# Kernel optimization log

Measured on AMD Instinct MI355X. Metric: run time of the kernel, lower is better.

Reference implementation:

```python
import jax, jax.numpy as jnp
import numpy as np

EMBED_DIM = 1024
NUM_HEADS = 16
HEAD_DIM = EMBED_DIM // NUM_HEADS


def setup_inputs() -> dict:
    key = jax.random.key(0)
    ks = jax.random.split(key, 11)
    B, S, D = 2, 2048, EMBED_DIM
    s = 1.0 / np.sqrt(D)
    inp = {
        "query": jax.random.normal(ks[0], (B, S, D), jnp.float32),
        "key": jax.random.normal(ks[1], (B, S, D), jnp.float32),
        "value": jax.random.normal(ks[2], (B, S, D), jnp.float32),
        # torch Linear weights: [out, in]
        "Wq": jax.random.normal(ks[3], (D, D), jnp.float32) * s,
        "bq": jnp.zeros((D,), jnp.float32),
        "Wk": jax.random.normal(ks[4], (D, D), jnp.float32) * s,
        "bk": jnp.zeros((D,), jnp.float32),
        "Wv": jax.random.normal(ks[5], (D, D), jnp.float32) * s,
        "bv": jnp.zeros((D,), jnp.float32),
        "Wo": jax.random.normal(ks[6], (D, D), jnp.float32) * s,
        "bo": jnp.zeros((D,), jnp.float32),
    }
    return inp


def reference(query, key, value, Wq, bq, Wk, bk, Wv, bv, Wo, bo):
    B, Q, D = query.shape
    K = key.shape[1]
    H, Hd = NUM_HEADS, HEAD_DIM
    # NOTE: source divides by scaling = head_dim**-0.5, i.e. multiplies by sqrt(head_dim)
    scaling = float(Hd) ** (-0.5)

    q = (query @ Wq.T + bq).reshape(B, Q, H, Hd).transpose(0, 2, 1, 3)  # [B,H,Q,Hd]
    k = (key @ Wk.T + bk).reshape(B, K, H, Hd).transpose(0, 2, 1, 3)    # [B,H,K,Hd]
    v = (value @ Wv.T + bv).reshape(B, K, H, Hd).transpose(0, 2, 1, 3)  # [B,H,K,Hd]

    scores = jnp.einsum("bhqd,bhkd->bhqk", q, k) / scaling
    attn = jax.nn.softmax(scores, axis=-1)  # dropout=0 (eval)
    out = jnp.einsum("bhqk,bhkd->bhqd", attn, v)
    out = out.transpose(0, 2, 1, 3).reshape(B, Q, D)
    return out @ Wo.T + bo
```

## Files before the change

kernel.cpp:

```cpp
#include <hip/hip_runtime.h>
#include <type_traits>
#include <utility>

#define B_ 2
#define S_ 2048
#define D_ 1024
#define H_ 16
#define HD_ 64
#define KDIM 1024

typedef __attribute__((ext_vector_type(8))) short    s16x8;
typedef __attribute__((ext_vector_type(8))) _Float16 h16x8;
typedef __attribute__((ext_vector_type(4))) float    f32x4;
typedef __attribute__((ext_vector_type(4))) int      i32x4;
typedef __attribute__((ext_vector_type(2))) int      i32x2;

template <typename T, typename = void> struct mfma_takes : std::false_type {};
template <typename T>
struct mfma_takes<T, std::void_t<decltype(__builtin_amdgcn_mfma_f32_16x16x32_f16(
    std::declval<T>(), std::declval<T>(), std::declval<f32x4>(), 0, 0, 0))>>
    : std::true_type {};
using frag8 = std::conditional_t<mfma_takes<h16x8>::value, h16x8, s16x8>;

__device__ __forceinline__ f32x4 mfma_f16(frag8 a, frag8 b, f32x4 c) {
  return __builtin_amdgcn_mfma_f32_16x16x32_f16(a, b, c, 0, 0, 0);
}

__device__ __forceinline__ short f2h(float f) {
  _Float16 h = (_Float16)f;
  short s; __builtin_memcpy(&s, &h, 2);
  return s;
}
__device__ __forceinline__ frag8 ld_frag(const short* p) {
  return __builtin_bit_cast(frag8, *(const i32x4*)p);
}
__device__ __forceinline__ float fast_exp2(float x) {
  return __builtin_amdgcn_exp2f(x);
}

typedef __attribute__((address_space(1))) const void gvoid;
typedef __attribute__((address_space(3))) void lvoid;
__device__ __forceinline__ void async_copy16(const void* g, void* l) {
  __builtin_amdgcn_global_load_lds((gvoid*)g, (lvoid*)l, 16, 0, 0);
}

#define RAW_BARRIER() asm volatile("s_barrier" ::: "memory")
#define WAITCNT_VM(n) asm volatile("s_waitcnt vmcnt(" #n ")" ::: "memory")

__global__ __launch_bounds__(256)
void conv_all(const float* __restrict__ q, const float* __restrict__ k,
              const float* __restrict__ v, const float* __restrict__ Wq,
              const float* __restrict__ Wk, const float* __restrict__ Wv,
              const float* __restrict__ Wo,
              short* __restrict__ qh, short* __restrict__ kh,
              short* __restrict__ vh, short* __restrict__ wq,
              short* __restrict__ wk, short* __restrict__ wv,
              short* __restrict__ wo) {
  const int blk = blockIdx.x;
  const float* src; short* dst; int base;
  if (blk < 2048)      { src = q;  dst = qh; base = blk; }
  else if (blk < 4096) { src = k;  dst = kh; base = blk - 2048; }
  else if (blk < 6144) { src = v;  dst = vh; base = blk - 4096; }
  else if (blk < 6656) { src = Wq; dst = wq; base = blk - 6144; }
  else if (blk < 7168) { src = Wk; dst = wk; base = blk - 6656; }
  else if (blk < 7680) { src = Wv; dst = wv; base = blk - 7168; }
  else                 { src = Wo; dst = wo; base = blk - 7680; }
  const int i = base * 2048 + threadIdx.x * 8;
  float4 a0 = *(const float4*)(src + i);
  float4 a1 = *(const float4*)(src + i + 4);
  short h[8] = { f2h(a0.x), f2h(a0.y), f2h(a0.z), f2h(a0.w),
                 f2h(a1.x), f2h(a1.y), f2h(a1.z), f2h(a1.w) };
  i32x4 ph; __builtin_memcpy(&ph, h, 16);
  *(i32x4*)(dst + i) = ph;
}

template <int OUTK>
__device__ __forceinline__
void gemm_body(const short* __restrict__ Ap, const short* __restrict__ Wp,
               const float* __restrict__ bias, void* __restrict__ Out,
               float scale, int omode, short* As, short* Bs, int bm, int bn) {
  const int t = threadIdx.x, wave = t >> 6, lane = t & 63;
  const int laneN = lane & 15, quad = lane >> 4;
  const int wm = wave & 1, wn = wave >> 1;

  f32x4 acc[4][4];
#pragma unroll
  for (int i = 0; i < 4; ++i)
#pragma unroll
    for (int j = 0; j < 4; ++j)
#pragma unroll
      for (int r = 0; r < 4; ++r) acc[i][j][r] = 0.f;

  auto stage = [&](int buf, int kk) {
#pragma unroll
    for (int j = 0; j < 2; ++j) {
      const int chunk = j * 256 + t;
      const int row = chunk >> 2;
      const int g = (chunk & 3) ^ ((row >> 1) & 3);
      async_copy16(Ap + (size_t)(bm * 128 + row) * KDIM + kk + g * 8,
                   As + buf * 4096 + chunk * 8);
      async_copy16(Wp + (size_t)(bn * 128 + row) * KDIM + kk + g * 8,
                   Bs + buf * 4096 + chunk * 8);
    }
  };

  stage(0, 0);
  int buf = 0;
  for (int kk = 0; kk < KDIM; kk += 32, buf ^= 1) {
    if (kk + 32 < KDIM) {
      stage(buf ^ 1, kk + 32);
      WAITCNT_VM(4);
    } else {
      WAITCNT_VM(0);
    }
    RAW_BARRIER();

    frag8 aF[4], bF[4];
#pragma unroll
    for (int mi = 0; mi < 4; ++mi) {
      const int row = wm * 64 + mi * 16 + laneN;
      aF[mi] = ld_frag(As + buf * 4096 + row * 32 +
                       ((quad ^ ((row >> 1) & 3)) * 8));
    }
#pragma unroll
    for (int ni = 0; ni < 4; ++ni) {
      const int row = wn * 64 + ni * 16 + laneN;
      bF[ni] = ld_frag(Bs + buf * 4096 + row * 32 +
                       ((quad ^ ((row >> 1) & 3)) * 8));
    }
#pragma unroll
    for (int mi = 0; mi < 4; ++mi)
#pragma unroll
      for (int ni = 0; ni < 4; ++ni)
        acc[mi][ni] = mfma_f16(aF[mi], bF[ni], acc[mi][ni]);
    RAW_BARRIER();
  }

#pragma unroll
  for (int mi = 0; mi < 4; ++mi)
#pragma unroll
    for (int ni = 0; ni < 4; ++ni) {
      const int colg = bn * 128 + wn * 64 + ni * 16 + laneN;
      const float bb = bias[colg];
      if (OUTK == 1 && omode == 2) {
        const int rowg0 = bm * 128 + wm * 64 + mi * 16 + quad * 4;
        const int b = rowg0 >> 11, s0 = rowg0 & 2047;
        const int h = colg >> 6, hd = colg & 63;
        short pk[4];
#pragma unroll
        for (int r = 0; r < 4; ++r) pk[r] = f2h(acc[mi][ni][r] + bb);
        i32x2 w; __builtin_memcpy(&w, pk, 8);
        *(i32x2*)((short*)Out + (((size_t)(b * H_ + h)) * HD_ + hd) * S_ + s0) = w;
      } else {
#pragma unroll
        for (int r = 0; r < 4; ++r) {
          const int rowg = bm * 128 + wm * 64 + mi * 16 + quad * 4 + r;
          const float v = acc[mi][ni][r] + bb;
          if (OUTK == 0) {
            ((float*)Out)[(size_t)rowg * 1024 + colg] = v;
          } else {
            const int b = rowg >> 11, s = rowg & 2047;
            const int h = colg >> 6, hd = colg & 63;
            ((short*)Out)[(((size_t)(b * H_ + h)) * S_ + s) * HD_ + hd] =
                f2h(v * scale);
          }
        }
      }
    }
}

__global__ __launch_bounds__(256, 3)
void gemm_qkv(const short* __restrict__ qh, const short* __restrict__ kh,
              const short* __restrict__ vh, const short* __restrict__ wq,
              const short* __restrict__ wk, const short* __restrict__ wv,
              const float* __restrict__ bq, const float* __restrict__ bk,
              const float* __restrict__ bv, short* __restrict__ Qf,
              short* __restrict__ Kf, short* __restrict__ Vt, float QS) {
  __shared__ short As[2 * 4096];
  __shared__ short Bs[2 * 4096];
  const int z = blockIdx.z;
  const short* A = z == 0 ? qh : z == 1 ? kh : vh;
  const short* W = z == 0 ? wq : z == 1 ? wk : wv;
  const float* bias = z == 0 ? bq : z == 1 ? bk : bv;
  short* Out = z == 0 ? Qf : z == 1 ? Kf : Vt;
  gemm_body<1>(A, W, bias, Out, z == 0 ? QS : 1.0f, z == 2 ? 2 : 1,
               As, Bs, blockIdx.y, blockIdx.x);
}

__global__ __launch_bounds__(256, 3)
void gemm_out(const short* __restrict__ Ow, const short* __restrict__ wo,
              const float* __restrict__ bo, float* __restrict__ out) {
  __shared__ short As[2 * 4096];
  __shared__ short Bs[2 * 4096];
  gemm_body<0>(Ow, wo, bo, out, 1.0f, 0, As, Bs, blockIdx.y, blockIdx.x);
}

__global__ __launch_bounds__(512, 2)
void attn(const short* __restrict__ Qf, const short* __restrict__ Kf,
          const short* __restrict__ Vt_, short* __restrict__ Ow) {
  __shared__ short Ks[2 * 4096];
  __shared__ short Vts[2 * 4096];
  __shared__ short Ps[8][16 * 72];

  const int qt = blockIdx.x, h = blockIdx.y, b = blockIdx.z;
  const size_t head = ((size_t)b * H_ + h) * (size_t)S_ * HD_;

  const int t = threadIdx.x;
  const int wave = t >> 6, lane = t & 63;
  const int laneN = lane & 15, quad = lane >> 4;

  frag8 qf[2];
  {
    const size_t row = (size_t)qt * 128 + wave * 16 + laneN;
#pragma unroll
    for (int half = 0; half < 2; ++half)
      qf[half] = ld_frag(Qf + head + row * HD_ + half * 32 + quad * 8);
  }

  f32x4 o[4];
  float m_r = -1e30f, l_r = 0.f;
#pragma unroll
  for (int i = 0; i < 4; ++i)
#pragma unroll
    for (int j = 0; j < 4; ++j) o[i][j] = 0.f;

  auto stage = [&](int buf, int kt) {
    const int chunk = t;
    const int row = chunk >> 3;
    const int g = (chunk & 7) ^ (row & 7);
    const int ldsoff = buf * 4096 + chunk * 8;
    async_copy16(Kf + head + (size_t)(kt * 64 + row) * HD_ + g * 8, Ks + ldsoff);
    async_copy16(Vt_ + head + (size_t)row * S_ + kt * 64 + g * 8, Vts + ldsoff);
  };

  stage(0, 0);
  int buf = 0;
  for (int kt = 0; kt < 32; ++kt, buf ^= 1) {
    if (kt + 1 < 32) {
      stage(buf ^ 1, kt + 1);
      WAITCNT_VM(2);
    } else {
      WAITCNT_VM(0);
    }
    RAW_BARRIER();

    frag8 vf[4][2];
#pragma unroll
    for (int dt = 0; dt < 4; ++dt) {
      const int row = dt * 16 + laneN;
#pragma unroll
      for (int half = 0; half < 2; ++half)
        vf[dt][half] = ld_frag(Vts + buf * 4096 + row * 64 +
                               (((half * 4 + quad) ^ (row & 7)) * 8));
    }

    f32x4 s[4];
#pragma unroll
    for (int nt = 0; nt < 4; ++nt) {
      const int row = nt * 16 + laneN;
      const int o0 = buf * 4096 + row * 64 + ((quad ^ (row & 7)) * 8);
      const int o1 = buf * 4096 + row * 64 + (((quad + 4) ^ (row & 7)) * 8);
      frag8 k0 = ld_frag(Ks + o0), k1 = ld_frag(Ks + o1);
      f32x4 acc;
#pragma unroll
      for (int j = 0; j < 4; ++j) acc[j] = 0.f;
      acc = mfma_f16(k0, qf[0], acc);
      acc = mfma_f16(k1, qf[1], acc);
      s[nt] = acc;
    }

    {
      float mx = -1e30f;
#pragma unroll
      for (int nt = 0; nt < 4; ++nt)
#pragma unroll
        for (int r = 0; r < 4; ++r) mx = fmaxf(mx, s[nt][r]);
      mx = fmaxf(mx, __shfl_xor(mx, 16));
      mx = fmaxf(mx, __shfl_xor(mx, 32));
      const float mn = fmaxf(m_r, mx);
      const float al = fast_exp2(m_r - mn);
      m_r = mn;
      float rs = 0.f;
#pragma unroll
      for (int nt = 0; nt < 4; ++nt)
#pragma unroll
        for (int r = 0; r < 4; ++r) {
          const float p = fast_exp2(s[nt][r] - mn);
          s[nt][r] = p; rs += p;
        }
      rs += __shfl_xor(rs, 16);
      rs += __shfl_xor(rs, 32);
      l_r = l_r * al + rs;
#pragma unroll
      for (int dt = 0; dt < 4; ++dt)
#pragma unroll
        for (int r = 0; r < 4; ++r) o[dt][r] *= al;
    }

#pragma unroll
    for (int nt = 0; nt < 4; ++nt) {
      short pk[4] = { f2h(s[nt][0]), f2h(s[nt][1]),
                      f2h(s[nt][2]), f2h(s[nt][3]) };
      i32x2 w; __builtin_memcpy(&w, pk, 8);
      *(i32x2*)&Ps[wave][laneN * 72 + nt * 16 + quad * 4] = w;
    }
    const frag8 p0 = ld_frag(&Ps[wave][laneN * 72 + quad * 8]);
    const frag8 p1 = ld_frag(&Ps[wave][laneN * 72 + 32 + quad * 8]);
#pragma unroll
    for (int dt = 0; dt < 4; ++dt) {
      o[dt] = mfma_f16(vf[dt][0], p0, o[dt]);
      o[dt] = mfma_f16(vf[dt][1], p1, o[dt]);
    }
    RAW_BARRIER();
  }

  {
    const float inv = 1.0f / l_r;
    const int sg = qt * 128 + wave * 16 + laneN;
    short* dst = Ow + ((size_t)b * S_ + sg) * D_ + h * HD_;
#pragma unroll
    for (int dt = 0; dt < 4; ++dt) {
      short pk[4] = { f2h(o[dt][0] * inv), f2h(o[dt][1] * inv),
                      f2h(o[dt][2] * inv), f2h(o[dt][3] * inv) };
      i32x2 w; __builtin_memcpy(&w, pk, 8);
      *(i32x2*)(dst + dt * 16 + quad * 4) = w;
    }
  }
}

extern "C" void kernel_launch(void* const* d_in, const int* in_sizes, int n_in,
                              void* d_out, int out_size, void* d_ws, size_t ws_size,
                              hipStream_t stream) {
  const float* q  = (const float*)d_in[0];
  const float* k  = (const float*)d_in[1];
  const float* v  = (const float*)d_in[2];
  const float* Wq = (const float*)d_in[3];
  const float* bq = (const float*)d_in[4];
  const float* Wk = (const float*)d_in[5];
  const float* bk = (const float*)d_in[6];
  const float* Wv = (const float*)d_in[7];
  const float* bv = (const float*)d_in[8];
  const float* Wo = (const float*)d_in[9];
  const float* bo = (const float*)d_in[10];

  const size_t NTOK = (size_t)B_ * S_ * D_;
  const size_t NW   = (size_t)D_ * D_;
  short* p = (short*)d_ws;
  short* qh = p; p += NTOK;  short* kh = p; p += NTOK;  short* vh = p; p += NTOK;
  short* wq = p; p += NW;    short* wk = p; p += NW;
  short* wv = p; p += NW;    short* wo = p; p += NW;
  short* Qf = p; p += NTOK;  short* Kf = p; p += NTOK;
  short* Vt = p; p += NTOK;  short* Ow = p; p += NTOK;

  dim3 blk(256);

  conv_all<<<8192, blk, 0, stream>>>(q, k, v, Wq, Wk, Wv, Wo,
                                     qh, kh, vh, wq, wk, wv, wo);

  const float QS = 11.541560327111707f;
  dim3 gqkv(D_ / 128, (B_ * S_) / 128, 3);
  gemm_qkv<<<gqkv, blk, 0, stream>>>(qh, kh, vh, wq, wk, wv, bq, bk, bv,
                                     Qf, Kf, Vt, QS);

  attn<<<dim3(S_ / 128, H_, B_), dim3(512), 0, stream>>>(Qf, Kf, Vt, Ow);

  dim3 gg(D_ / 128, (B_ * S_) / 128);
  gemm_out<<<gg, blk, 0, stream>>>(Ow, wo, bo, (float*)d_out);
}
```

Baseline: 234.8 us.

## Fuse fp32-to-fp16 activation conversion into QKV GEMM and remap attention blocks per XCD

Measured after the change: 246.6 us. 1.05x slower.

```diff
diff --git a/kernel.cpp b/kernel.cpp
--- a/kernel.cpp
+++ b/kernel.cpp
@@ -34,6 +34,11 @@
 __device__ __forceinline__ frag8 ld_frag(const short* p) {
   return __builtin_bit_cast(frag8, *(const i32x4*)p);
 }
+__device__ __forceinline__ frag8 cvt_frag(f32x4 a, f32x4 b) {
+  _Float16 h[8] = { (_Float16)a[0], (_Float16)a[1], (_Float16)a[2], (_Float16)a[3],
+                    (_Float16)b[0], (_Float16)b[1], (_Float16)b[2], (_Float16)b[3] };
+  frag8 f; __builtin_memcpy(&f, h, 16); return f;
+}
 __device__ __forceinline__ float fast_exp2(float x) {
   return __builtin_amdgcn_exp2f(x);
 }
@@ -48,23 +53,16 @@
 #define WAITCNT_VM(n) asm volatile("s_waitcnt vmcnt(" #n ")" ::: "memory")
 
 __global__ __launch_bounds__(256)
-void conv_all(const float* __restrict__ q, const float* __restrict__ k,
-              const float* __restrict__ v, const float* __restrict__ Wq,
-              const float* __restrict__ Wk, const float* __restrict__ Wv,
-              const float* __restrict__ Wo,
-              short* __restrict__ qh, short* __restrict__ kh,
-              short* __restrict__ vh, short* __restrict__ wq,
-              short* __restrict__ wk, short* __restrict__ wv,
-              short* __restrict__ wo) {
+void conv_w(const float* __restrict__ Wq, const float* __restrict__ Wk,
+            const float* __restrict__ Wv, const float* __restrict__ Wo,
+            short* __restrict__ wq, short* __restrict__ wk,
+            short* __restrict__ wv, short* __restrict__ wo) {
   const int blk = blockIdx.x;
   const float* src; short* dst; int base;
-  if (blk < 2048)      { src = q;  dst = qh; base = blk; }
-  else if (blk < 4096) { src = k;  dst = kh; base = blk - 2048; }
-  else if (blk < 6144) { src = v;  dst = vh; base = blk - 4096; }
-  else if (blk < 6656) { src = Wq; dst = wq; base = blk - 6144; }
-  else if (blk < 7168) { src = Wk; dst = wk; base = blk - 6656; }
-  else if (blk < 7680) { src = Wv; dst = wv; base = blk - 7168; }
-  else                 { src = Wo; dst = wo; base = blk - 7680; }
+  if (blk < 512)       { src = Wq; dst = wq; base = blk; }
+  else if (blk < 1024) { src = Wk; dst = wk; base = blk - 512; }
+  else if (blk < 1536) { src = Wv; dst = wv; base = blk - 1024; }
+  else                 { src = Wo; dst = wo; base = blk - 1536; }
   const int i = base * 2048 + threadIdx.x * 8;
   float4 a0 = *(const float4*)(src + i);
   float4 a1 = *(const float4*)(src + i + 4);
@@ -74,11 +72,124 @@
   *(i32x4*)(dst + i) = ph;
 }
 
-template <int OUTK>
-__device__ __forceinline__
-void gemm_body(const short* __restrict__ Ap, const short* __restrict__ Wp,
-               const float* __restrict__ bias, void* __restrict__ Out,
-               float scale, int omode, short* As, short* Bs, int bm, int bn) {
+__global__ __launch_bounds__(256, 3)
+void gemm_qkv(const float* __restrict__ qa, const float* __restrict__ ka,
+              const float* __restrict__ va, const short* __restrict__ wq,
+              const short* __restrict__ wk, const short* __restrict__ wv,
+              const float* __restrict__ bq, const float* __restrict__ bk,
+              const float* __restrict__ bv, short* __restrict__ Qf,
+              short* __restrict__ Kf, short* __restrict__ Vt, float QS) {
+  __shared__ float Asf[2 * 4096];
+  __shared__ short Bs[2 * 4096];
+
+  const int z = blockIdx.z;
+  const float* Ap = z == 0 ? qa : z == 1 ? ka : va;
+  const short* Wp = z == 0 ? wq : z == 1 ? wk : wv;
+  const float* bias = z == 0 ? bq : z == 1 ? bk : bv;
+  short* Out = z == 0 ? Qf : z == 1 ? Kf : Vt;
+  const float scale = z == 0 ? QS : 1.0f;
+  const int omode = z == 2 ? 2 : 1;
+  const int bm = blockIdx.y, bn = blockIdx.x;
+
+  const int t = threadIdx.x, wave = t >> 6, lane = t & 63;
+  const int laneN = lane & 15, quad = lane >> 4;
+  const int wm = wave & 1, wn = wave >> 1;
+
+  f32x4 acc[4][4];
+#pragma unroll
+  for (int i = 0; i < 4; ++i)
+#pragma unroll
+    for (int j = 0; j < 4; ++j)
+#pragma unroll
+      for (int r = 0; r < 4; ++r) acc[i][j][r] = 0.f;
+
+  auto stage = [&](int buf, int kk) {
+#pragma unroll
+    for (int j = 0; j < 4; ++j) {
+      const int chunk = j * 256 + t;
+      const int row = chunk >> 3;
+      const int g = (chunk & 7) ^ (row & 7);
+      async_copy16(Ap + (size_t)(bm * 128 + row) * KDIM + kk + g * 4,
+                   Asf + buf * 4096 + chunk * 4);
+    }
+#pragma unroll
+    for (int j = 0; j < 2; ++j) {
+      const int chunk = j * 256 + t;
+      const int row = chunk >> 2;
+      const int g = (chunk & 3) ^ ((row >> 1) & 3);
+      async_copy16(Wp + (size_t)(bn * 128 + row) * KDIM + kk + g * 8,
+                   Bs + buf * 4096 + chunk * 8);
+    }
+  };
+
+  stage(0, 0);
+  int buf = 0;
+  for (int kk = 0; kk < KDIM; kk += 32, buf ^= 1) {
+    if (kk + 32 < KDIM) {
+      stage(buf ^ 1, kk + 32);
+      WAITCNT_VM(6);
+    } else {
+      WAITCNT_VM(0);
+    }
+    RAW_BARRIER();
+
+    frag8 aF[4], bF[4];
+#pragma unroll
+    for (int mi = 0; mi < 4; ++mi) {
+      const int row = wm * 64 + mi * 16 + laneN;
+      const float* rp = Asf + buf * 4096 + row * 32;
+      f32x4 a0 = *(const f32x4*)(rp + (((quad * 2) ^ (row & 7)) * 4));
+      f32x4 a1 = *(const f32x4*)(rp + (((quad * 2 + 1) ^ (row & 7)) * 4));
+      aF[mi] = cvt_frag(a0, a1);
+    }
+#pragma unroll
+    for (int ni = 0; ni < 4; ++ni) {
+      const int row = wn * 64 + ni * 16 + laneN;
+      bF[ni] = ld_frag(Bs + buf * 4096 + row * 32 +
+                       ((quad ^ ((row >> 1) & 3)) * 8));
+    }
+#pragma unroll
+    for (int mi = 0; mi < 4; ++mi)
+#pragma unroll
+      for (int ni = 0; ni < 4; ++ni)
+        acc[mi][ni] = mfma_f16(aF[mi], bF[ni], acc[mi][ni]);
+    RAW_BARRIER();
+  }
+
+#pragma unroll
+  for (int mi = 0; mi < 4; ++mi)
+#pragma unroll
+    for (int ni = 0; ni < 4; ++ni) {
+      const int colg = bn * 128 + wn * 64 + ni * 16 + laneN;
+      const float bb = bias[colg];
+      if (omode == 2) {
+        const int rowg0 = bm * 128 + wm * 64 + mi * 16 + quad * 4;
+        const int b = rowg0 >> 11, s0 = rowg0 & 2047;
+        const int h = colg >> 6, hd = colg & 63;
+        short pk[4];
+#pragma unroll
+        for (int r = 0; r < 4; ++r) pk[r] = f2h(acc[mi][ni][r] + bb);
+        i32x2 w; __builtin_memcpy(&w, pk, 8);
+        *(i32x2*)(Out + (((size_t)(b * H_ + h)) * HD_ + hd) * S_ + s0) = w;
+      } else {
+#pragma unroll
+        for (int r = 0; r < 4; ++r) {
+          const int rowg = bm * 128 + wm * 64 + mi * 16 + quad * 4 + r;
+          const int b = rowg >> 11, s = rowg & 2047;
+          const int h = colg >> 6, hd = colg & 63;
+          Out[(((size_t)(b * H_ + h)) * S_ + s) * HD_ + hd] =
+              f2h((acc[mi][ni][r] + bb) * scale);
+        }
+      }
+    }
+}
+
+__global__ __launch_bounds__(256, 3)
+void gemm_out(const short* __restrict__ Ap, const short* __restrict__ Wp,
+              const float* __restrict__ bias, float* __restrict__ Out) {
+  __shared__ short As[2 * 4096];
+  __shared__ short Bs[2 * 4096];
+  const int bm = blockIdx.y, bn = blockIdx.x;
   const int t = threadIdx.x, wave = t >> 6, lane = t & 63;
   const int laneN = lane & 15, quad = lane >> 4;
   const int wm = wave & 1, wn = wave >> 1;
@@ -142,57 +253,12 @@
     for (int ni = 0; ni < 4; ++ni) {
       const int colg = bn * 128 + wn * 64 + ni * 16 + laneN;
       const float bb = bias[colg];
-      if (OUTK == 1 && omode == 2) {
-        const int rowg0 = bm * 128 + wm * 64 + mi * 16 + quad * 4;
-        const int b = rowg0 >> 11, s0 = rowg0 & 2047;
-        const int h = colg >> 6, hd = colg & 63;
-        short pk[4];
-#pragma unroll
-        for (int r = 0; r < 4; ++r) pk[r] = f2h(acc[mi][ni][r] + bb);
-        i32x2 w; __builtin_memcpy(&w, pk, 8);
-        *(i32x2*)((short*)Out + (((size_t)(b * H_ + h)) * HD_ + hd) * S_ + s0) = w;
-      } else {
-#pragma unroll
-        for (int r = 0; r < 4; ++r) {
-          const int rowg = bm * 128 + wm * 64 + mi * 16 + quad * 4 + r;
-          const float v = acc[mi][ni][r] + bb;
-          if (OUTK == 0) {
-            ((float*)Out)[(size_t)rowg * 1024 + colg] = v;
-          } else {
-            const int b = rowg >> 11, s = rowg & 2047;
-            const int h = colg >> 6, hd = colg & 63;
-            ((short*)Out)[(((size_t)(b * H_ + h)) * S_ + s) * HD_ + hd] =
-                f2h(v * scale);
-          }
-        }
+#pragma unroll
+      for (int r = 0; r < 4; ++r) {
+        const int rowg = bm * 128 + wm * 64 + mi * 16 + quad * 4 + r;
+        Out[(size_t)rowg * 1024 + colg] = acc[mi][ni][r] + bb;
       }
     }
-}
-
-__global__ __launch_bounds__(256, 3)
-void gemm_qkv(const short* __restrict__ qh, const short* __restrict__ kh,
-              const short* __restrict__ vh, const short* __restrict__ wq,
-              const short* __restrict__ wk, const short* __restrict__ wv,
-              const float* __restrict__ bq, const float* __restrict__ bk,
-              const float* __restrict__ bv, short* __restrict__ Qf,
-              short* __restrict__ Kf, short* __restrict__ Vt, float QS) {
-  __shared__ short As[2 * 4096];
-  __shared__ short Bs[2 * 4096];
-  const int z = blockIdx.z;
-  const short* A = z == 0 ? qh : z == 1 ? kh : vh;
-  const short* W = z == 0 ? wq : z == 1 ? wk : wv;
-  const float* bias = z == 0 ? bq : z == 1 ? bk : bv;
-  short* Out = z == 0 ? Qf : z == 1 ? Kf : Vt;
-  gemm_body<1>(A, W, bias, Out, z == 0 ? QS : 1.0f, z == 2 ? 2 : 1,
-               As, Bs, blockIdx.y, blockIdx.x);
-}
-
-__global__ __launch_bounds__(256, 3)
-void gemm_out(const short* __restrict__ Ow, const short* __restrict__ wo,
-              const float* __restrict__ bo, float* __restrict__ out) {
-  __shared__ short As[2 * 4096];
-  __shared__ short Bs[2 * 4096];
-  gemm_body<0>(Ow, wo, bo, out, 1.0f, 0, As, Bs, blockIdx.y, blockIdx.x);
 }
 
 __global__ __launch_bounds__(512, 2)
@@ -202,7 +268,10 @@
   __shared__ short Vts[2 * 4096];
   __shared__ short Ps[8][16 * 72];
 
-  const int qt = blockIdx.x, h = blockIdx.y, b = blockIdx.z;
+  const int blk = blockIdx.x;
+  const int xcd = blk & 7, local = blk >> 3;
+  const int pair = xcd * 4 + (local >> 4);
+  const int h = pair & 15, b = pair >> 4, qt = local & 15;
   const size_t head = ((size_t)b * H_ + h) * (size_t)S_ * HD_;
 
   const int t = threadIdx.x;
@@ -346,7 +415,6 @@
   const size_t NTOK = (size_t)B_ * S_ * D_;
   const size_t NW   = (size_t)D_ * D_;
   short* p = (short*)d_ws;
-  short* qh = p; p += NTOK;  short* kh = p; p += NTOK;  short* vh = p; p += NTOK;
   short* wq = p; p += NW;    short* wk = p; p += NW;
   short* wv = p; p += NW;    short* wo = p; p += NW;
   short* Qf = p; p += NTOK;  short* Kf = p; p += NTOK;
@@ -354,15 +422,14 @@
 
   dim3 blk(256);
 
-  conv_all<<<8192, blk, 0, stream>>>(q, k, v, Wq, Wk, Wv, Wo,
-                                     qh, kh, vh, wq, wk, wv, wo);
+  conv_w<<<2048, blk, 0, stream>>>(Wq, Wk, Wv, Wo, wq, wk, wv, wo);
 
   const float QS = 11.541560327111707f;
   dim3 gqkv(D_ / 128, (B_ * S_) / 128, 3);
-  gemm_qkv<<<gqkv, blk, 0, stream>>>(qh, kh, vh, wq, wk, wv, bq, bk, bv,
+  gemm_qkv<<<gqkv, blk, 0, stream>>>(q, k, v, wq, wk, wv, bq, bk, bv,
                                      Qf, Kf, Vt, QS);
 
-  attn<<<dim3(S_ / 128, H_, B_), dim3(512), 0, stream>>>(Qf, Kf, Vt, Ow);
+  attn<<<dim3(512), dim3(512), 0, stream>>>(Qf, Kf, Vt, Ow);
 
   dim3 gg(D_ / 128, (B_ * S_) / 128);
   gemm_out<<<gg, blk, 0, stream>>>(Ow, wo, bo, (float*)d_out);
```
